# Performance work log

Measured on AMD Instinct MI355X. Metric: run time of the kernel, lower is better.

The kernel has to match this reference:

```python
import jax, jax.numpy as jnp
import numpy as np

B, S, D, H = 2, 2048, 1024, 16
HEAD_DIM = D // H
THETA = 10000.0


def setup_inputs() -> dict:
    key = jax.random.key(0)
    kx, kq, kk, kv, ko = jax.random.split(key, 5)
    w_scale = jnp.float32(D ** -0.5)  # keep logits O(1)
    return {
        "x": jax.random.normal(kx, (B, S, D), dtype=jnp.float32),
        "WQ": jax.random.normal(kq, (D, D), dtype=jnp.float32) * w_scale,
        "WK": jax.random.normal(kk, (D, D), dtype=jnp.float32) * w_scale,
        "WV": jax.random.normal(kv, (D, D), dtype=jnp.float32) * w_scale,
        "WO": jax.random.normal(ko, (D, D), dtype=jnp.float32) * w_scale,
        "token_positions": jnp.arange(S, dtype=jnp.int32),
    }


def _rope(x, pos, theta):
    # x: [B, H, S, dh]; pos: [S]. Interleaved (even, odd) pair rotation.
    dh = x.shape[-1]
    inv_freq = theta ** (-jnp.arange(0, dh, 2, dtype=jnp.float32) / dh)  # [dh/2]
    ang = pos.astype(jnp.float32)[:, None] * inv_freq                    # [S, dh/2]
    cos, sin = jnp.cos(ang), jnp.sin(ang)
    x1, x2 = x[..., 0::2], x[..., 1::2]
    r1 = x1 * cos - x2 * sin
    r2 = x1 * sin + x2 * cos
    return jnp.stack([r1, r2], axis=-1).reshape(x.shape)


def reference(x, WQ, WK, WV, WO, token_positions):
    Bs, Ss, Dm = x.shape
    dh = Dm // H
    # QKV projections (Linear with no bias, y = x @ W.T), split heads -> [B,H,S,dh]
    q = (x @ WQ.T).reshape(Bs, Ss, H, dh).transpose(0, 2, 1, 3)
    k = (x @ WK.T).reshape(Bs, Ss, H, dh).transpose(0, 2, 1, 3)
    v = (x @ WV.T).reshape(Bs, Ss, H, dh).transpose(0, 2, 1, 3)
    q = _rope(q, token_positions, THETA)
    k = _rope(k, token_positions, THETA)
    scores = jnp.einsum("bhqd,bhkd->bhqk", q, k) * jnp.float32(dh ** -0.5)
    causal = jnp.tril(jnp.ones((Ss, Ss), dtype=bool))
    scores = jnp.where(causal, scores, jnp.finfo(scores.dtype).min)
    attn = jax.nn.softmax(scores, axis=-1)
    out = jnp.einsum("bhqk,bhkd->bhqd", attn, v)
    out = out.transpose(0, 2, 1, 3).reshape(Bs, Ss, Dm)
    return out @ WO.T
```

## Files before the change

kernel.cpp:

```cpp
#include <hip/hip_runtime.h>
#include <hip/hip_bf16.h>


#define S_LEN 2048
#define NHEADS 16
#define NEG_SENT -30000.0f

typedef __attribute__((ext_vector_type(8))) short short8;
typedef __attribute__((ext_vector_type(4))) float f32x4;
typedef unsigned int u32;
typedef unsigned short u16;

static __device__ __forceinline__ float bf2f(u16 u) {
  union { u32 i; float f; } v; v.i = ((u32)u) << 16; return v.f;
}
static __device__ __forceinline__ u16 f2bf(float f) {
  union { float f; u32 i; } v; v.f = f;
  u32 u = v.i;
  u32 r = (u + 0x7fffu + ((u >> 16) & 1u)) >> 16;
  return (u16)r;
}
static __device__ __forceinline__ u32 cvtpk(float a, float b) {
  u32 r;
  asm("v_cvt_pk_bf16_f32 %0, %1, %2" : "=v"(r) : "v"(a), "v"(b));
  return r;
}

static __device__ __forceinline__ void glds16(const void* g, void* l) {
  __builtin_amdgcn_global_load_lds((const __attribute__((address_space(1))) u32*)g,
                                   (__attribute__((address_space(3))) u32*)l, 16, 0, 0);
}

__global__ void convert_kernel(const float* __restrict__ x, const float* __restrict__ wq,
                               const float* __restrict__ wk, const float* __restrict__ wv,
                               const float* __restrict__ wo, u16* __restrict__ xb,
                               u16* __restrict__ wb) {
  int i = blockIdx.x * blockDim.x + threadIdx.x;
  const float* src; u16* dst; int off;
  if (i < 1048576) { src = x; dst = xb; off = i; }
  else {
    int j = i - 1048576;
    int widx = j >> 18;
    off = j & 262143;
    src = (widx == 0) ? wq : (widx == 1) ? wk : (widx == 2) ? wv : wo;
    dst = wb + (size_t)widx * 1048576;
  }
  float4 v = ((const float4*)src)[off];
  ushort4 o;
  o.x = f2bf(v.x); o.y = f2bf(v.y); o.z = f2bf(v.z); o.w = f2bf(v.w);
  ((ushort4*)dst)[off] = o;
}

__global__ void rope_kernel(u32* __restrict__ Qb, u32* __restrict__ Kb,
                            const int* __restrict__ pos) {
  int i = blockIdx.x * blockDim.x + threadIdx.x;
  int c = i & 511;
  int rowi = i >> 9;
  int s = rowi & (S_LEN - 1);
  int ip = c & 31;
  float p = (float)pos[s];
  float ang = p * __builtin_exp2f((float)ip * -0.41524101186f);
  float sn, cs;
  sincosf(ang, &sn, &cs);
  u32 v = Qb[i];
  float x1 = bf2f((u16)(v & 0xffff)), x2 = bf2f((u16)(v >> 16));
  float r1 = x1 * cs - x2 * sn, r2 = x1 * sn + x2 * cs;
  Qb[i] = (u32)f2bf(r1) | ((u32)f2bf(r2) << 16);
  v = Kb[i];
  x1 = bf2f((u16)(v & 0xffff)); x2 = bf2f((u16)(v >> 16));
  r1 = x1 * cs - x2 * sn; r2 = x1 * sn + x2 * cs;
  Kb[i] = (u32)f2bf(r1) | ((u32)f2bf(r2) << 16);
}

template <int OUTMODE>
__global__ __launch_bounds__(256, 2) void gemm_bt(const u16* __restrict__ A,
                                                  const u16* __restrict__ B,
                                                  u16* __restrict__ o0, u16* __restrict__ o1,
                                                  u16* __restrict__ o2, float* __restrict__ oF,
                                                  int K) {
  __shared__ __align__(16) u16 AsBs[2 * 128 * 64];
  u16* const As = AsBs;
  u16* const Bs = AsBs + 128 * 64;
  const int tid = threadIdx.x, w = tid >> 6, l = tid & 63, l15 = l & 15, l4 = l >> 4;
  const int wr = w >> 1, wc = w & 1;
  const int m0 = blockIdx.y << 7, n0 = blockIdx.x << 7;
  const int r = tid >> 3;
  const int swcol = ((tid & 7) << 4) ^ ((r & 7) << 4);
  const char* Ag = (const char*)A + (((size_t)(m0 + r) * K) << 1) + swcol;
  const char* Bg = (const char*)B + (((size_t)(n0 + r) * K) << 1) + swcol;
  char* AsW = (char*)As + (w << 10);
  char* BsW = (char*)Bs + (w << 10);
  const size_t rowskip = ((size_t)32 * K) << 1;
  f32x4 acc[4][4] = {};
  for (int k0 = 0; k0 < K; k0 += 64) {
    __syncthreads();
    const size_t kb = (size_t)k0 << 1;
#pragma unroll
    for (int i = 0; i < 4; i++) {
      glds16(Ag + kb + (size_t)i * rowskip, AsW + i * 4096);
      glds16(Bg + kb + (size_t)i * rowskip, BsW + i * 4096);
    }
    __syncthreads();
#pragma unroll
    for (int kk = 0; kk < 2; kk++) {
      short8 a[4], b[4];
#pragma unroll
      for (int m = 0; m < 4; m++) {
        int row = (wr << 6) + (m << 4) + l15;
        a[m] = *(const short8*)((const char*)As + row * 128 +
                                (((kk << 6) + (l4 << 4)) ^ ((row & 7) << 4)));
      }
#pragma unroll
      for (int n = 0; n < 4; n++) {
        int row = (wc << 6) + (n << 4) + l15;
        b[n] = *(const short8*)((const char*)Bs + row * 128 +
                                (((kk << 6) + (l4 << 4)) ^ ((row & 7) << 4)));
      }
#pragma unroll
      for (int m = 0; m < 4; m++)
#pragma unroll
        for (int n = 0; n < 4; n++)
          acc[m][n] = __builtin_amdgcn_mfma_f32_16x16x32_bf16(a[m], b[n], acc[m][n], 0, 0, 0);
    }
  }
  if (OUTMODE == 0 && n0 >= 2048) {
    __syncthreads();
    u16* T = AsBs;
#pragma unroll
    for (int m = 0; m < 4; m++)
#pragma unroll
      for (int n = 0; n < 4; n++) {
        int ct = (wc << 6) + (n << 4) + l15;
#pragma unroll
        for (int j = 0; j < 4; j++) {
          int rt = (wr << 6) + (m << 4) + (l4 << 2) + j;
          T[rt * 128 + (ct ^ (((rt >> 6) & 1) << 1))] = f2bf(acc[m][n][j]);
        }
      }
    __syncthreads();
    const int d = tid >> 1, sh = tid & 1;
    const int dr = d ^ (sh << 1);
    const int bb = m0 >> 11;
    const int colv = (n0 & 1023) + d;
    const int row = (((bb << 4) | (colv >> 6)) << 6) | (colv & 63);
    u16* dst = o2 + ((size_t)row << 11) + (m0 & (S_LEN - 1)) + (sh << 6);
#pragma unroll
    for (int k8 = 0; k8 < 8; k8++) {
      u16 tmp[8];
#pragma unroll
      for (int e = 0; e < 8; e++) tmp[e] = T[((sh << 6) + (k8 << 3) + e) * 128 + dr];
      *(uint4*)(dst + (k8 << 3)) = *(const uint4*)tmp;
    }
    return;
  }
#pragma unroll
  for (int m = 0; m < 4; m++) {
    int grow_b = m0 + (wr << 6) + (m << 4) + (l4 << 2);
#pragma unroll
    for (int n = 0; n < 4; n++) {
      int gcol = n0 + (wc << 6) + (n << 4) + l15;
#pragma unroll
      for (int j = 0; j < 4; j++) {
        int grow = grow_b + j;
        float v = acc[m][n][j];
        if (OUTMODE == 0) {
          u16* base = (gcol < 1024) ? o0 : o1;
          base[((size_t)grow << 10) + (gcol & 1023)] = f2bf(v);
        } else {
          oF[((size_t)grow << 10) + gcol] = v;
        }
      }
    }
  }
}

__global__ __launch_bounds__(512, 1) void attn_kernel(const u16* __restrict__ Q,
                                                      const u16* __restrict__ K,
                                                      const u16* __restrict__ Vt,
                                                      u16* __restrict__ O) {
  extern __shared__ __align__(16) char smem[];
  const int tid = threadIdx.x, w = tid >> 6, l = tid & 63, l15 = l & 15, g = l >> 4;
  const int grp = w >> 2, w4 = w & 3;
  const int i = blockIdx.x;
  const int xcd = i & 7, slot = i >> 3;
  const int bh = ((slot >> 3) << 3) | xcd;
  const int p = slot & 7;
  const int b = bh >> 4, h = bh & 15;
  const float C2 = 0.125f * 1.44269504089f;
  const int swz = (l15 & 7) << 4;

  const int gt = tid & 255;
  const int r = gt >> 3;
  const int swc = ((gt & 7) << 4) ^ ((r & 7) << 4);
  const char* Kg = (const char*)K + ((size_t)(b * S_LEN + r) << 11) + (h << 7) + swc;
  const char* Vg = (const char*)Vt + ((size_t)((bh << 6) + r) << 12) + swc;
  char* const KsG = smem + (grp << 15);
  char* const VsG = smem + (grp << 15) + 16384;
  char* const Pw = smem + 65536 + (w << 11);
  float* const oMrg = (float*)smem;
  float* const mlMrg = (float*)(smem + 65536);

#define STAGE(T, BSEL)                                              \
  do {                                                              \
    char* kd = KsG + ((BSEL) << 13) + (w4 << 10);                   \
    char* vd = VsG + ((BSEL) << 13) + (w4 << 10);                   \
    const char* ks = Kg + ((size_t)(T) << 17);                      \
    const char* vs = Vg + ((T) << 7);                               \
    glds16(ks, kd);                                                 \
    glds16(ks + (32 << 11), kd + 4096);                             \
    glds16(vs, vd);                                                 \
    glds16(vs + ((size_t)32 << 12), vd + 4096);                     \
  } while (0)

  auto run_qt = [&](int qt) {
    const int q0 = qt << 7;
    const int nr = qt + 1;

    short8 aQ[2][2];
    {
      const int qrow0 = q0 + (w4 << 5) + l15;
      const u16* qp = Q + (((size_t)(b * S_LEN + qrow0)) << 10) + (h << 6) + (g << 3);
      aQ[0][0] = *(const short8*)qp;
      aQ[0][1] = *(const short8*)(qp + 32);
      aQ[1][0] = *(const short8*)(qp + (16 << 10));
      aQ[1][1] = *(const short8*)(qp + (16 << 10) + 32);
    }
    f32x4 o[2][4] = {};
    float m_r[2] = {NEG_SENT, NEG_SENT}, l_r[2] = {0.f, 0.f};

    STAGE(grp, 0);
    __syncthreads();

    for (int rr = 0; rr < nr; ++rr) {
      const int bsel = rr & 1;
      if (rr + 1 < nr) STAGE(2 * (rr + 1) + grp, bsel ^ 1);
      const char* Kbuf = KsG + (bsel << 13);
      const char* Vbuf = VsG + (bsel << 13);
      const int t = 2 * rr + grp;
      const bool domask = (rr == nr - 1);

      f32x4 s[2][4] = {};
#pragma unroll
      for (int kk = 0; kk < 2; ++kk) {
        short8 aK[4];
#pragma unroll
        for (int n = 0; n < 4; ++n) {
          int row = (n << 4) + l15;
          aK[n] = *(const short8*)(Kbuf + row * 128 + (((kk << 6) + (g << 4)) ^ swz));
        }
        __builtin_amdgcn_s_setprio(1);
#pragma unroll
        for (int n = 0; n < 4; ++n) {
          s[0][n] = __builtin_amdgcn_mfma_f32_16x16x32_bf16(aK[n], aQ[0][kk], s[0][n], 0, 0, 0);
          s[1][n] = __builtin_amdgcn_mfma_f32_16x16x32_bf16(aK[n], aQ[1][kk], s[1][n], 0, 0, 0);
        }
        __builtin_amdgcn_s_setprio(0);
      }
      if (domask) {
#pragma unroll
        for (int qs = 0; qs < 2; ++qs) {
          int qg = q0 + (w4 << 5) + (qs << 4) + l15;
#pragma unroll
          for (int n = 0; n < 4; ++n)
#pragma unroll
            for (int jj = 0; jj < 4; ++jj) {
              int key = (t << 6) + (n << 4) + (g << 2) + jj;
              if (key > qg) s[qs][n][jj] = NEG_SENT;
            }
        }
      }
      float mx2[2];
#pragma unroll
      for (int qs = 0; qs < 2; ++qs) {
        float mx = s[qs][0][0];
#pragma unroll
        for (int n = 0; n < 4; ++n)
#pragma unroll
          for (int jj = 0; jj < 4; ++jj) mx = fmaxf(mx, s[qs][n][jj]);
        mx = fmaxf(mx, __shfl_xor(mx, 16));
        mx = fmaxf(mx, __shfl_xor(mx, 32));
        mx2[qs] = mx;
      }
      if (!__all((mx2[0] - m_r[0] <= 44.f) & (mx2[1] - m_r[1] <= 44.f))) {
        float fac[2];
#pragma unroll
        for (int qs = 0; qs < 2; ++qs) {
          float mn = fmaxf(m_r[qs], mx2[qs]);
          float fc = __builtin_exp2f((m_r[qs] - mn) * C2);
          m_r[qs] = mn;
          l_r[qs] *= fc;
          fac[qs] = fc;
        }
#pragma unroll
        for (int qs = 0; qs < 2; ++qs)
#pragma unroll
          for (int jj = 0; jj < 4; ++jj) {
            float fo = __shfl(fac[qs], (g << 2) + jj, 16);
#pragma unroll
            for (int nd = 0; nd < 4; ++nd) o[qs][nd][jj] *= fo;
          }
      }
      short8 aP[2][2];
#pragma unroll
      for (int qs = 0; qs < 2; ++qs) {
        float mC = m_r[qs] * C2;
        float rs = 0.f;
        u32 pk[8];
#pragma unroll
        for (int n = 0; n < 4; ++n) {
          float p0 = __builtin_exp2f(s[qs][n][0] * C2 - mC);
          float p1 = __builtin_exp2f(s[qs][n][1] * C2 - mC);
          float p2 = __builtin_exp2f(s[qs][n][2] * C2 - mC);
          float p3 = __builtin_exp2f(s[qs][n][3] * C2 - mC);
          rs += (p0 + p1) + (p2 + p3);
          pk[2 * n] = cvtpk(p0, p1);
          pk[2 * n + 1] = cvtpk(p2, p3);
        }
        rs += __shfl_xor(rs, 16);
        rs += __shfl_xor(rs, 32);
        l_r[qs] += rs;
        char* pr = Pw + l15 * 128;
#pragma unroll
        for (int n = 0; n < 4; ++n) {
          uint2 pv;
          pv.x = pk[2 * n];
          pv.y = pk[2 * n + 1];
          *(uint2*)(pr + (((n << 5) + (g << 3)) ^ swz)) = pv;
        }
#pragma unroll
        for (int kk = 0; kk < 2; ++kk)
          aP[qs][kk] = *(const short8*)(Pw + l15 * 128 + ((((kk << 6) + (g << 4))) ^ swz));
      }
#pragma unroll
      for (int kk = 0; kk < 2; ++kk) {
        int co = (kk << 6) + (g << 4);
        __builtin_amdgcn_s_setprio(1);
#pragma unroll
        for (int nd = 0; nd < 4; ++nd) {
          int row = (nd << 4) + l15;
          short8 bV = *(const short8*)(Vbuf + row * 128 + (co ^ swz));
          o[0][nd] = __builtin_amdgcn_mfma_f32_16x16x32_bf16(aP[0][kk], bV, o[0][nd], 0, 0, 0);
          o[1][nd] = __builtin_amdgcn_mfma_f32_16x16x32_bf16(aP[1][kk], bV, o[1][nd], 0, 0, 0);
        }
        __builtin_amdgcn_s_setprio(0);
      }
      __syncthreads();
    }

    if (grp == 1) {
      float* ob = oMrg + (w4 << 11);
#pragma unroll
      for (int qs = 0; qs < 2; ++qs)
#pragma unroll
        for (int nd = 0; nd < 4; ++nd)
          *(f32x4*)(ob + (((qs << 2) | nd) << 8) + (l << 2)) = o[qs][nd];
      float* mb = mlMrg + (w4 << 8);
      mb[l] = m_r[0];
      mb[64 + l] = m_r[1];
      mb[128 + l] = l_r[0];
      mb[192 + l] = l_r[1];
    }
    __syncthreads();
    if (grp == 0) {
      float* ob = oMrg + (w4 << 11);
      float* mb = mlMrg + (w4 << 8);
#pragma unroll
      for (int qs = 0; qs < 2; ++qs) {
        float mB = mb[(qs << 6) + l];
        float lB = mb[128 + (qs << 6) + l];
        float mS = fmaxf(m_r[qs], mB);
        float fA = __builtin_exp2f((m_r[qs] - mS) * C2);
        float fB = __builtin_exp2f((mB - mS) * C2);
        float linv = 1.f / (l_r[qs] * fA + lB * fB);
        float sA = fA * linv, sB = fB * linv;
        f32x4 oB[4];
#pragma unroll
        for (int nd = 0; nd < 4; ++nd)
          oB[nd] = *(const f32x4*)(ob + (((qs << 2) | nd) << 8) + (l << 2));
#pragma unroll
        for (int jj = 0; jj < 4; ++jj) {
          float sAo = __shfl(sA, (g << 2) + jj, 16);
          float sBo = __shfl(sB, (g << 2) + jj, 16);
          int qg = q0 + (w4 << 5) + (qs << 4) + (g << 2) + jj;
          u16* orow = O + (((size_t)(b * S_LEN + qg)) << 10) + (h << 6) + l15;
#pragma unroll
          for (int nd = 0; nd < 4; ++nd)
            orow[nd << 4] = f2bf(o[qs][nd][jj] * sAo + oB[nd][jj] * sBo);
        }
      }
    }
    __syncthreads();
  };

  run_qt(p);
  run_qt(15 - p);
#undef STAGE
}

extern "C" void kernel_launch(void* const* d_in, const int* in_sizes, int n_in,
                              void* d_out, int out_size, void* d_ws, size_t ws_size,
                              hipStream_t stream) {
  (void)in_sizes; (void)n_in; (void)out_size; (void)ws_size;
  const float* x = (const float*)d_in[0];
  const float* wq = (const float*)d_in[1];
  const float* wk = (const float*)d_in[2];
  const float* wv = (const float*)d_in[3];
  const float* wo = (const float*)d_in[4];
  const int* pos = (const int*)d_in[5];
  char* ws = (char*)d_ws;
  u16* xb = (u16*)ws;
  u16* wb = (u16*)(ws + ((size_t)8 << 20));
  u16* Qb = (u16*)(ws + ((size_t)16 << 20));
  u16* Kb = (u16*)(ws + ((size_t)24 << 20));
  u16* Vtg = (u16*)(ws + ((size_t)32 << 20));
  u16* Ab = (u16*)(ws + ((size_t)40 << 20));
  float* out = (float*)d_out;

  convert_kernel<<<8192, 256, 0, stream>>>(x, wq, wk, wv, wo, xb, wb);
  dim3 g1(24, 32);
  gemm_bt<0><<<g1, 256, 0, stream>>>(xb, wb, Qb, Kb, Vtg, nullptr, 1024);
  rope_kernel<<<8192, 256, 0, stream>>>((u32*)Qb, (u32*)Kb, pos);
  attn_kernel<<<256, 512, 81920, stream>>>(Qb, Kb, Vtg, Ab);
  dim3 g3(8, 32);
  gemm_bt<1><<<g3, 256, 0, stream>>>(Ab, wb + (size_t)3 * 1048576, nullptr, nullptr, nullptr,
                                     out, 1024);
}
```

Measured before the change: 114.1 us.

## Restructure attention into 256-thread blocks over 64-row query tiles without KV split

The attention kernel moves from 512-thread blocks, where two wave groups split the key range for a 128-row query tile and merge partial softmax states through shared memory, to 256-thread blocks that each handle a 64-row query tile over the full key range. Each wave now owns 16 query rows. The grid doubles to 512 blocks with half the shared memory, so two blocks can share a CU, and the final merge step disappears. In exchange, each K/V tile staged into shared memory is reused by half as many query rows, and per-block causal work is less even.

```diff
diff --git a/kernel.cpp b/kernel.cpp
--- a/kernel.cpp
+++ b/kernel.cpp
@@ -3,7 +3,6 @@
 
 
 #define S_LEN 2048
-#define NHEADS 16
 #define NEG_SENT -30000.0f
 
 typedef __attribute__((ext_vector_type(8))) short short8;
@@ -174,36 +173,33 @@
   }
 }
 
-__global__ __launch_bounds__(512, 1) void attn_kernel(const u16* __restrict__ Q,
+__global__ __launch_bounds__(256, 2) void attn_kernel(const u16* __restrict__ Q,
                                                       const u16* __restrict__ K,
                                                       const u16* __restrict__ Vt,
                                                       u16* __restrict__ O) {
   extern __shared__ __align__(16) char smem[];
   const int tid = threadIdx.x, w = tid >> 6, l = tid & 63, l15 = l & 15, g = l >> 4;
-  const int grp = w >> 2, w4 = w & 3;
   const int i = blockIdx.x;
-  const int xcd = i & 7, slot = i >> 3;
+  const int c = i & 255;
+  const int xcd = c & 7, slot = c >> 3;
   const int bh = ((slot >> 3) << 3) | xcd;
-  const int p = slot & 7;
+  const int u0 = (slot & 7) | ((i >> 8) << 3);
   const int b = bh >> 4, h = bh & 15;
   const float C2 = 0.125f * 1.44269504089f;
   const int swz = (l15 & 7) << 4;
 
-  const int gt = tid & 255;
-  const int r = gt >> 3;
-  const int swc = ((gt & 7) << 4) ^ ((r & 7) << 4);
+  const int r = tid >> 3;
+  const int swc = ((tid & 7) << 4) ^ ((r & 7) << 4);
   const char* Kg = (const char*)K + ((size_t)(b * S_LEN + r) << 11) + (h << 7) + swc;
   const char* Vg = (const char*)Vt + ((size_t)((bh << 6) + r) << 12) + swc;
-  char* const KsG = smem + (grp << 15);
-  char* const VsG = smem + (grp << 15) + 16384;
-  char* const Pw = smem + 65536 + (w << 11);
-  float* const oMrg = (float*)smem;
-  float* const mlMrg = (float*)(smem + 65536);
+  char* const Ks = smem;
+  char* const Vs = smem + 16384;
+  char* const Pw = smem + 32768 + (w << 11);
 
 #define STAGE(T, BSEL)                                              \
   do {                                                              \
-    char* kd = KsG + ((BSEL) << 13) + (w4 << 10);                   \
-    char* vd = VsG + ((BSEL) << 13) + (w4 << 10);                   \
+    char* kd = Ks + ((BSEL) << 13) + (w << 10);                     \
+    char* vd = Vs + ((BSEL) << 13) + (w << 10);                     \
     const char* ks = Kg + ((size_t)(T) << 17);                      \
     const char* vs = Vg + ((T) << 7);                               \
     glds16(ks, kd);                                                 \
@@ -212,34 +208,30 @@
     glds16(vs + ((size_t)32 << 12), vd + 4096);                     \
   } while (0)
 
-  auto run_qt = [&](int qt) {
-    const int q0 = qt << 7;
-    const int nr = qt + 1;
-
-    short8 aQ[2][2];
+  auto run_u = [&](int u) {
+    const int q0 = u << 6;
+    const int nr = u + 1;
+
+    short8 aQ[2];
     {
-      const int qrow0 = q0 + (w4 << 5) + l15;
+      const int qrow0 = q0 + (w << 4) + l15;
       const u16* qp = Q + (((size_t)(b * S_LEN + qrow0)) << 10) + (h << 6) + (g << 3);
-      aQ[0][0] = *(const short8*)qp;
-      aQ[0][1] = *(const short8*)(qp + 32);
-      aQ[1][0] = *(const short8*)(qp + (16 << 10));
-      aQ[1][1] = *(const short8*)(qp + (16 << 10) + 32);
-    }
-    f32x4 o[2][4] = {};
-    float m_r[2] = {NEG_SENT, NEG_SENT}, l_r[2] = {0.f, 0.f};
-
-    STAGE(grp, 0);
-    __syncthreads();
-
-    for (int rr = 0; rr < nr; ++rr) {
-      const int bsel = rr & 1;
-      if (rr + 1 < nr) STAGE(2 * (rr + 1) + grp, bsel ^ 1);
-      const char* Kbuf = KsG + (bsel << 13);
-      const char* Vbuf = VsG + (bsel << 13);
-      const int t = 2 * rr + grp;
-      const bool domask = (rr == nr - 1);
-
-      f32x4 s[2][4] = {};
+      aQ[0] = *(const short8*)qp;
+      aQ[1] = *(const short8*)(qp + 32);
+    }
+    f32x4 o[4] = {};
+    float m_r = NEG_SENT, l_r = 0.f;
+
+    STAGE(0, 0);
+    __syncthreads();
+
+    for (int t = 0; t < nr; ++t) {
+      const int bsel = t & 1;
+      if (t + 1 < nr) STAGE(t + 1, bsel ^ 1);
+      const char* Kbuf = Ks + (bsel << 13);
+      const char* Vbuf = Vs + (bsel << 13);
+
+      f32x4 s[4] = {};
 #pragma unroll
       for (int kk = 0; kk < 2; ++kk) {
         short8 aK[4];
@@ -250,75 +242,57 @@
         }
         __builtin_amdgcn_s_setprio(1);
 #pragma unroll
-        for (int n = 0; n < 4; ++n) {
-          s[0][n] = __builtin_amdgcn_mfma_f32_16x16x32_bf16(aK[n], aQ[0][kk], s[0][n], 0, 0, 0);
-          s[1][n] = __builtin_amdgcn_mfma_f32_16x16x32_bf16(aK[n], aQ[1][kk], s[1][n], 0, 0, 0);
-        }
+        for (int n = 0; n < 4; ++n)
+          s[n] = __builtin_amdgcn_mfma_f32_16x16x32_bf16(aK[n], aQ[kk], s[n], 0, 0, 0);
         __builtin_amdgcn_s_setprio(0);
       }
-      if (domask) {
-#pragma unroll
-        for (int qs = 0; qs < 2; ++qs) {
-          int qg = q0 + (w4 << 5) + (qs << 4) + l15;
-#pragma unroll
-          for (int n = 0; n < 4; ++n)
-#pragma unroll
-            for (int jj = 0; jj < 4; ++jj) {
-              int key = (t << 6) + (n << 4) + (g << 2) + jj;
-              if (key > qg) s[qs][n][jj] = NEG_SENT;
-            }
-        }
-      }
-      float mx2[2];
-#pragma unroll
-      for (int qs = 0; qs < 2; ++qs) {
-        float mx = s[qs][0][0];
+      if (t == nr - 1) {
+        const int qg = q0 + (w << 4) + l15;
 #pragma unroll
         for (int n = 0; n < 4; ++n)
 #pragma unroll
-          for (int jj = 0; jj < 4; ++jj) mx = fmaxf(mx, s[qs][n][jj]);
-        mx = fmaxf(mx, __shfl_xor(mx, 16));
-        mx = fmaxf(mx, __shfl_xor(mx, 32));
-        mx2[qs] = mx;
-      }
-      if (!__all((mx2[0] - m_r[0] <= 44.f) & (mx2[1] - m_r[1] <= 44.f))) {
-        float fac[2];
-#pragma unroll
-        for (int qs = 0; qs < 2; ++qs) {
-          float mn = fmaxf(m_r[qs], mx2[qs]);
-          float fc = __builtin_exp2f((m_r[qs] - mn) * C2);
-          m_r[qs] = mn;
-          l_r[qs] *= fc;
-          fac[qs] = fc;
-        }
-#pragma unroll
-        for (int qs = 0; qs < 2; ++qs)
-#pragma unroll
           for (int jj = 0; jj < 4; ++jj) {
-            float fo = __shfl(fac[qs], (g << 2) + jj, 16);
-#pragma unroll
-            for (int nd = 0; nd < 4; ++nd) o[qs][nd][jj] *= fo;
+            int key = (t << 6) + (n << 4) + (g << 2) + jj;
+            if (key > qg) s[n][jj] = NEG_SENT;
           }
       }
-      short8 aP[2][2];
-#pragma unroll
-      for (int qs = 0; qs < 2; ++qs) {
-        float mC = m_r[qs] * C2;
+      float mx = s[0][0];
+#pragma unroll
+      for (int n = 0; n < 4; ++n)
+#pragma unroll
+        for (int jj = 0; jj < 4; ++jj) mx = fmaxf(mx, s[n][jj]);
+      mx = fmaxf(mx, __shfl_xor(mx, 16));
+      mx = fmaxf(mx, __shfl_xor(mx, 32));
+      if (!__all(mx - m_r <= 44.f)) {
+        float mn = fmaxf(m_r, mx);
+        float fc = __builtin_exp2f((m_r - mn) * C2);
+        m_r = mn;
+        l_r *= fc;
+#pragma unroll
+        for (int jj = 0; jj < 4; ++jj) {
+          float fo = __shfl(fc, (g << 2) + jj, 16);
+#pragma unroll
+          for (int nd = 0; nd < 4; ++nd) o[nd][jj] *= fo;
+        }
+      }
+      short8 aP[2];
+      {
+        float mC = m_r * C2;
         float rs = 0.f;
         u32 pk[8];
 #pragma unroll
         for (int n = 0; n < 4; ++n) {
-          float p0 = __builtin_exp2f(s[qs][n][0] * C2 - mC);
-          float p1 = __builtin_exp2f(s[qs][n][1] * C2 - mC);
-          float p2 = __builtin_exp2f(s[qs][n][2] * C2 - mC);
-          float p3 = __builtin_exp2f(s[qs][n][3] * C2 - mC);
+          float p0 = __builtin_exp2f(s[n][0] * C2 - mC);
+          float p1 = __builtin_exp2f(s[n][1] * C2 - mC);
+          float p2 = __builtin_exp2f(s[n][2] * C2 - mC);
+          float p3 = __builtin_exp2f(s[n][3] * C2 - mC);
           rs += (p0 + p1) + (p2 + p3);
           pk[2 * n] = cvtpk(p0, p1);
           pk[2 * n + 1] = cvtpk(p2, p3);
         }
         rs += __shfl_xor(rs, 16);
         rs += __shfl_xor(rs, 32);
-        l_r[qs] += rs;
+        l_r += rs;
         char* pr = Pw + l15 * 128;
 #pragma unroll
         for (int n = 0; n < 4; ++n) {
@@ -329,7 +303,7 @@
         }
 #pragma unroll
         for (int kk = 0; kk < 2; ++kk)
-          aP[qs][kk] = *(const short8*)(Pw + l15 * 128 + ((((kk << 6) + (g << 4))) ^ swz));
+          aP[kk] = *(const short8*)(pr + (((kk << 6) + (g << 4)) ^ swz));
       }
 #pragma unroll
       for (int kk = 0; kk < 2; ++kk) {
@@ -339,61 +313,25 @@
         for (int nd = 0; nd < 4; ++nd) {
           int row = (nd << 4) + l15;
           short8 bV = *(const short8*)(Vbuf + row * 128 + (co ^ swz));
-          o[0][nd] = __builtin_amdgcn_mfma_f32_16x16x32_bf16(aP[0][kk], bV, o[0][nd], 0, 0, 0);
-          o[1][nd] = __builtin_amdgcn_mfma_f32_16x16x32_bf16(aP[1][kk], bV, o[1][nd], 0, 0, 0);
+          o[nd] = __builtin_amdgcn_mfma_f32_16x16x32_bf16(aP[kk], bV, o[nd], 0, 0, 0);
         }
         __builtin_amdgcn_s_setprio(0);
       }
       __syncthreads();
     }
-
-    if (grp == 1) {
-      float* ob = oMrg + (w4 << 11);
-#pragma unroll
-      for (int qs = 0; qs < 2; ++qs)
-#pragma unroll
-        for (int nd = 0; nd < 4; ++nd)
-          *(f32x4*)(ob + (((qs << 2) | nd) << 8) + (l << 2)) = o[qs][nd];
-      float* mb = mlMrg + (w4 << 8);
-      mb[l] = m_r[0];
-      mb[64 + l] = m_r[1];
-      mb[128 + l] = l_r[0];
-      mb[192 + l] = l_r[1];
-    }
-    __syncthreads();
-    if (grp == 0) {
-      float* ob = oMrg + (w4 << 11);
-      float* mb = mlMrg + (w4 << 8);
-#pragma unroll
-      for (int qs = 0; qs < 2; ++qs) {
-        float mB = mb[(qs << 6) + l];
-        float lB = mb[128 + (qs << 6) + l];
-        float mS = fmaxf(m_r[qs], mB);
-        float fA = __builtin_exp2f((m_r[qs] - mS) * C2);
-        float fB = __builtin_exp2f((mB - mS) * C2);
-        float linv = 1.f / (l_r[qs] * fA + lB * fB);
-        float sA = fA * linv, sB = fB * linv;
-        f32x4 oB[4];
-#pragma unroll
-        for (int nd = 0; nd < 4; ++nd)
-          oB[nd] = *(const f32x4*)(ob + (((qs << 2) | nd) << 8) + (l << 2));
-#pragma unroll
-        for (int jj = 0; jj < 4; ++jj) {
-          float sAo = __shfl(sA, (g << 2) + jj, 16);
-          float sBo = __shfl(sB, (g << 2) + jj, 16);
-          int qg = q0 + (w4 << 5) + (qs << 4) + (g << 2) + jj;
-          u16* orow = O + (((size_t)(b * S_LEN + qg)) << 10) + (h << 6) + l15;
-#pragma unroll
-          for (int nd = 0; nd < 4; ++nd)
-            orow[nd << 4] = f2bf(o[qs][nd][jj] * sAo + oB[nd][jj] * sBo);
-        }
-      }
-    }
-    __syncthreads();
+    float linv = 1.f / l_r;
+#pragma unroll
+    for (int jj = 0; jj < 4; ++jj) {
+      float lo = __shfl(linv, (g << 2) + jj, 16);
+      int qg = q0 + (w << 4) + (g << 2) + jj;
+      u16* orow = O + (((size_t)(b * S_LEN + qg)) << 10) + (h << 6) + l15;
+#pragma unroll
+      for (int nd = 0; nd < 4; ++nd) orow[nd << 4] = f2bf(o[nd][jj] * lo);
+    }
   };
 
-  run_qt(p);
-  run_qt(15 - p);
+  run_u(u0);
+  run_u(31 - u0);
 #undef STAGE
 }
 
@@ -420,7 +358,7 @@
   dim3 g1(24, 32);
   gemm_bt<0><<<g1, 256, 0, stream>>>(xb, wb, Qb, Kb, Vtg, nullptr, 1024);
   rope_kernel<<<8192, 256, 0, stream>>>((u32*)Qb, (u32*)Kb, pos);
-  attn_kernel<<<256, 512, 81920, stream>>>(Qb, Kb, Vtg, Ab);
+  attn_kernel<<<512, 256, 40960, stream>>>(Qb, Kb, Vtg, Ab);
   dim3 g3(8, 32);
   gemm_bt<1><<<g3, 256, 0, stream>>>(Ab, wb + (size_t)3 * 1048576, nullptr, nullptr, nullptr,
                                      out, 1024);
```

Measured after the change: 116.7 us. 2.3% more time.
